# Kernel optimization log

Measured on AMD Instinct MI355X. Metric: run time of the kernel, lower is better.

The kernel has to match this reference:

```python
import jax, jax.numpy as jnp
import numpy as np

N, S, V, DEG, K, HID = 4096, 128, 32, 32, 8, 64
E = N * DEG
LAMBDA_ATTN = 0.55


def setup_inputs():
    key = jax.random.key(0)
    ks = jax.random.split(key, 16)
    def w(k, shape, fan_in):
        return jax.random.normal(k, shape, jnp.float32) / np.float32(np.sqrt(fan_in))
    return {
        "h_s": jax.random.normal(ks[0], (N, S), jnp.float32),
        "h_v": jax.random.normal(ks[1], (N, V, 3), jnp.float32),
        "pos": jax.random.normal(ks[2], (N, 3), jnp.float32),
        "edge_index": jax.random.randint(ks[3], (2, E), 0, N),
        "batch": jnp.zeros((N,), jnp.int32),
        "W1": w(ks[4], (S, S), S),
        "Wg": w(ks[5], (S, 2 * V), S),
        "W2": w(ks[6], (S, S), S),
        "Wm1": w(ks[7], (S, HID), S), "bm1": jnp.zeros((HID,), jnp.float32),
        "Wm2": w(ks[8], (HID, 1), HID), "bm2": jnp.zeros((1,), jnp.float32),
        "Wq": w(ks[9], (S, S), S), "Wk": w(ks[10], (S, S), S),
        "Wa1": w(ks[11], (3 * S, S), 3 * S), "ba1": jnp.zeros((S,), jnp.float32),
        "Wa2": w(ks[12], (S, 1), S), "ba2": jnp.zeros((1,), jnp.float32),
    }


def _edge_feats(pos, src, dst):
    # vectors src - dst, length-expanded scalar attr [E,S], direction vector attr [E,V,3]
    vec = pos[src] - pos[dst]
    ln = jnp.linalg.norm(vec, axis=-1, keepdims=True)
    dirn = jnp.where(ln > 1e-12, vec / jnp.maximum(ln, 1e-12), 0.0)  # nan_to_num
    es = jnp.broadcast_to(ln, (src.shape[0], S))
    ev = jnp.broadcast_to(dirn[:, None, :], (src.shape[0], V, 3))
    return es, ev


def _scatter_softmax(scores, seg, n, validf):
    s = jnp.where(validf > 0, scores, -jnp.inf)
    mx = jax.ops.segment_max(s, seg, num_segments=n)
    mx = jnp.where(jnp.isfinite(mx), mx, 0.0)
    e = jnp.where(validf > 0, jnp.exp(s - mx[seg]), 0.0)
    den = jax.ops.segment_sum(e, seg, num_segments=n)
    return e / jnp.maximum(den[seg], 1e-9)


def _backbone(s, v, src, dst, es, ev, msg_mask, W1, Wg, W2):
    # gather-src gated messages, modulated by edge attrs, scatter-sum to dst
    m_s = jax.nn.relu(s[src] @ W1) * es                       # [E,S]
    g = s[src] @ Wg                                           # [E,2V]
    m_v = v[src] * g[:, :V, None] + ev * g[:, V:, None]       # [E,V,3]
    if msg_mask is not None:
        m_s = m_s * msg_mask[:, None]
        m_v = m_v * msg_mask[:, None, None]
    ds = jax.ops.segment_sum(m_s, dst, num_segments=N) @ W2
    dv = jax.ops.segment_sum(m_v, dst, num_segments=N)
    return ds, dv


def reference(h_s, h_v, pos, edge_index, batch, W1, Wg, W2, Wm1, bm1, Wm2, bm2, Wq, Wk, Wa1, ba1, Wa2, ba2):
    src, dst = edge_index[0], edge_index[1]
    # local message passing with residual
    es, ev = _edge_feats(pos, src, dst)
    ds, dv = _backbone(h_s, h_v, src, dst, es, ev, None, W1, Wg, W2)
    hl_s = h_s + ds
    hl_v = h_v + dv
    # master selection (soft score m, hard mask at 0.5)
    m = jax.nn.sigmoid((jax.nn.relu(hl_s @ Wm1 + bm1) @ Wm2 + bm2)[:, 0])
    mask = (m > 0.5).astype(hl_s.dtype)
    # virtual edge generation among master nodes (dense attention, thresholded)
    attn = jax.nn.sigmoid((hl_s @ Wq) @ (hl_s @ Wk).T / np.float32(np.sqrt(S)))  # [N,N]
    adj = jnp.zeros((N, N), hl_s.dtype).at[src, dst].add(1.0)
    mm = mask[:, None] * mask[None, :]
    allowed = (mm > 0) & (adj == 0) & (~jnp.eye(N, dtype=bool))
    vals, cols = jax.lax.top_k(jnp.where(allowed, attn, -jnp.inf), K)  # [N,K]
    vf = ((vals > LAMBDA_ATTN) & jnp.isfinite(vals)).astype(hl_s.dtype)
    rows = jnp.broadcast_to(jnp.arange(N)[:, None], (N, K))
    A_virtual = jnp.zeros((N, N), hl_s.dtype).at[rows, cols].add(vf)
    vsrc = rows.reshape(-1)
    vdst = cols.reshape(-1)
    vvf = vf.reshape(-1)
    # attention-based decay weights on virtual edges (scatter-softmax over dst)
    es_v, ev_v = _edge_feats(pos, vsrc, vdst)
    attn_in = jnp.concatenate([hl_s[vsrc], hl_s[vdst], es_v], axis=-1)  # [NK,3S]
    sc = (jax.nn.relu(attn_in @ Wa1 + ba1) @ Wa2 + ba2)[:, 0]
    decay = _scatter_softmax(sc, vdst, N, vvf)
    # hierarchical pass: induced master-master edges (w=1) + virtual edges (w=decay)
    asrc = jnp.concatenate([src, vsrc])
    adst = jnp.concatenate([dst, vdst])
    a_es = jnp.concatenate([es, es_v * decay[:, None]], axis=0)
    a_ev = jnp.concatenate([ev, ev_v * decay[:, None, None]], axis=0)
    amask = jnp.concatenate([mask[src] * mask[dst], vvf])
    dms, dmv = _backbone(hl_s, hl_v, asrc, adst, a_es, a_ev, amask, W1, Wg, W2)
    # expand hierarchical update to full node set (zero at non-masters), blend by m
    exp_s = mask[:, None] * (hl_s + dms)
    exp_v = mask[:, None, None] * (hl_v + dmv)
    hf_s = (1 - m[:, None]) * hl_s + m[:, None] * exp_s
    hf_v = (1 - m[:, None, None]) * hl_v + m[:, None, None] * exp_v
    return hf_s, hf_v, pos, A_virtual, m
```

## Files before the change

kernel.cpp:

```cpp
#include <hip/hip_runtime.h>
#include <math.h>

#define NN 4096
#define EE 131072
#define NKMAX 32768

#define SCALE_FX 8388608.0
#define INV_FX   (1.0/8388608.0)

__device__ __forceinline__ void atomAddFx(long long* p, float v) {
  atomicAdd((unsigned long long*)p, (unsigned long long)llrint((double)v * SCALE_FX));
}
__device__ __forceinline__ float fxToF(long long v) {
  return (float)((double)v * INV_FX);
}

#define OFF_LN    ((size_t)0)
#define OFF_DIRN  (OFF_LN + EE)
#define OFF_R     (OFF_DIRN + (size_t)EE*3)
#define OFF_G     (OFF_R + (size_t)NN*128)
#define OFF_P1    (OFF_G + (size_t)NN*64)
#define OFF_HLS   (OFF_P1 + (size_t)NN*96)
#define OFF_HLV   (OFF_HLS + (size_t)NN*128)
#define OFF_MVAL  (OFF_HLV + (size_t)NN*96)
#define OFF_MASK  (OFF_MVAL + NN)
#define OFF_Q     (OFF_MASK + NN)
#define OFF_K     (OFF_Q + (size_t)NN*128)
#define OFF_A1    (OFF_K + (size_t)NN*128)
#define OFF_A2    (OFF_A1 + (size_t)NN*128)
#define OFF_R2    (OFF_A2 + (size_t)NN*128)
#define OFF_G2    (OFF_R2 + (size_t)NN*128)
#define OFF_P2    (OFF_G2 + (size_t)NN*64)
#define OFF_W3    (OFF_P2 + (size_t)NN*96)
#define OFF_LNV   (OFF_W3 + 128)
#define OFF_DIRV  (OFF_LNV + NKMAX)
#define OFF_SC    (OFF_DIRV + (size_t)NKMAX*3)
#define OFF_EEXP  (OFF_SC + NKMAX)
#define OFF_VEDGE (OFF_EEXP + NKMAX)
#define OFF_MIDX  (OFF_VEDGE + (size_t)NKMAX*2)
#define OFF_PT    (OFF_MIDX + NN)
#define OFF_MEDGE (OFF_PT + (size_t)NN*32)
#define OFF_SF    (OFF_MEDGE + EE)
#define OFF_ZBEG  (OFF_SF + (size_t)NN*128)
#define OFF_ACCS  (OFF_ZBEG)
#define OFF_ACCV  (OFF_ACCS + (size_t)NN*256)
#define OFF_DEN64 (OFF_ACCV + (size_t)NN*192)
#define OFF_MX    (OFF_DEN64 + (size_t)NN*2)
#define OFF_ADJ   (OFF_MX + NN)
#define OFF_CNT   (OFF_ADJ + (size_t)NN*128)
#define OFF_END   (OFF_CNT + 64)

#define OUT_HFS 0
#define OUT_HFV 524288
#define OUT_POS 917504
#define OUT_AV  929792
#define OUT_M   17707008

#define INSERT8(TV, TC, VAL, IDX) do { \
  if ((VAL) > TV[7]) { \
    _Pragma("unroll") \
    for (int k_ = 7; k_ >= 1; --k_) { \
      bool gtk_ = (VAL) > TV[k_]; bool gtm_ = (VAL) > TV[k_-1]; \
      float nv_ = gtk_ ? (gtm_ ? TV[k_-1] : (VAL)) : TV[k_]; \
      int   ni_ = gtk_ ? (gtm_ ? TC[k_-1] : (IDX)) : TC[k_]; \
      TV[k_] = nv_; TC[k_] = ni_; } \
    bool gt0_ = (VAL) > TV[0]; \
    TV[0] = gt0_ ? (VAL) : TV[0]; TC[0] = gt0_ ? (IDX) : TC[0]; \
  } } while (0)

__device__ __forceinline__ void merge32(float (&tv)[8], int (&tc)[8]) {
  #pragma unroll
  for (int m = 1; m <= 16; m <<= 1) {
    float av[16]; int ac[16];
    #pragma unroll
    for (int k = 0; k < 8; ++k) { av[k] = tv[k]; ac[k] = tc[k]; }
    #pragma unroll
    for (int k = 0; k < 8; ++k) {
      av[8+k] = __shfl_xor(tv[7-k], m, 64);
      ac[8+k] = __shfl_xor(tc[7-k], m, 64);
    }
    #pragma unroll
    for (int d = 8; d >= 1; d >>= 1) {
      #pragma unroll
      for (int i = 0; i < 16; ++i) {
        if ((i & d) == 0) {
          const int jx = i + d;
          if (jx < 16) {
            bool sw = (av[i] < av[jx]) || (av[i] == av[jx] && ac[i] > ac[jx]);
            float t1 = sw ? av[jx] : av[i]; float t2 = sw ? av[i] : av[jx];
            int   u1 = sw ? ac[jx] : ac[i]; int   u2 = sw ? ac[i] : ac[jx];
            av[i] = t1; av[jx] = t2; ac[i] = u1; ac[jx] = u2;
          }
        }
      }
    }
    #pragma unroll
    for (int k = 0; k < 8; ++k) { tv[k] = av[k]; tc[k] = ac[k]; }
  }
}

__global__ void hmp_edge_prep(const int* __restrict__ ei, const float* __restrict__ pos,
                              float* __restrict__ ln, float* __restrict__ dirn,
                              unsigned long long* __restrict__ adj) {
  int e = blockIdx.x * 256 + threadIdx.x;
  if (e >= EE) return;
  int s = ei[e], d = ei[EE + e];
  float vx = pos[s*3+0] - pos[d*3+0];
  float vy = pos[s*3+1] - pos[d*3+1];
  float vz = pos[s*3+2] - pos[d*3+2];
  float l = sqrtf(vx*vx + vy*vy + vz*vz);
  ln[e] = l;
  if (l > 1e-12f) {
    dirn[e*3+0] = vx / l; dirn[e*3+1] = vy / l; dirn[e*3+2] = vz / l;
  } else {
    dirn[e*3+0] = 0.f; dirn[e*3+1] = 0.f; dirn[e*3+2] = 0.f;
  }
  atomicOr(&adj[(size_t)s*64 + (d >> 6)], 1ULL << (d & 63));
}

struct GemmJobs {
  const float* A;
  const float* W[6];
  float* C[6];
  int Nc[6];
  int act[6];
  const float* res;
  const float* mval;
  const float* maskf;
};

__global__ __launch_bounds__(256) void hmp_gemm_k128(GemmJobs P) {
  const int g = blockIdx.z;
  const int nc = P.Nc[g];
  if ((int)blockIdx.y * 64 >= nc) return;
  const float* __restrict__ W = P.W[g];
  float* __restrict__ C = P.C[g];
  const int act = P.act[g];
  __shared__ float As[32][68];
  __shared__ float Bs[32][64];
  const int tid = threadIdx.x;
  const int row0 = blockIdx.x * 64, col0 = blockIdx.y * 64;
  const int ty = tid >> 4, tx = tid & 15;
  float acc[4][4];
  #pragma unroll
  for (int i = 0; i < 4; ++i)
    #pragma unroll
    for (int j = 0; j < 4; ++j) acc[i][j] = 0.f;

  for (int kb = 0; kb < 4; ++kb) {
    #pragma unroll
    for (int q = 0; q < 2; ++q) {
      int f4 = tid + 256*q;
      int r = f4 >> 3, cg = f4 & 7;
      float4 av = *(const float4*)&P.A[(size_t)(row0+r)*128 + kb*32 + cg*4];
      As[cg*4+0][r] = av.x; As[cg*4+1][r] = av.y; As[cg*4+2][r] = av.z; As[cg*4+3][r] = av.w;
    }
    #pragma unroll
    for (int q = 0; q < 2; ++q) {
      int f4 = tid + 256*q;
      int kr = f4 >> 4, cg = f4 & 15;
      *(float4*)&Bs[kr][cg*4] = *(const float4*)&W[(size_t)(kb*32+kr)*nc + col0 + cg*4];
    }
    __syncthreads();
    #pragma unroll
    for (int kk = 0; kk < 32; ++kk) {
      float4 a = *(float4*)&As[kk][ty*4];
      float4 b = *(float4*)&Bs[kk][tx*4];
      acc[0][0] += a.x*b.x; acc[0][1] += a.x*b.y; acc[0][2] += a.x*b.z; acc[0][3] += a.x*b.w;
      acc[1][0] += a.y*b.x; acc[1][1] += a.y*b.y; acc[1][2] += a.y*b.z; acc[1][3] += a.y*b.w;
      acc[2][0] += a.z*b.x; acc[2][1] += a.z*b.y; acc[2][2] += a.z*b.z; acc[2][3] += a.z*b.w;
      acc[3][0] += a.w*b.x; acc[3][1] += a.w*b.y; acc[3][2] += a.w*b.z; acc[3][3] += a.w*b.w;
    }
    __syncthreads();
  }
  #pragma unroll
  for (int i = 0; i < 4; ++i) {
    int rr = row0 + ty*4 + i;
    float mv = 0.f, mk = 0.f;
    if (act == 3) { mv = P.mval[rr]; mk = P.maskf[rr]; }
    #pragma unroll
    for (int j = 0; j < 4; ++j) {
      int cc = col0 + tx*4 + j;
      float v = acc[i][j];
      if (act == 1) v = fmaxf(v, 0.f);
      else if (act == 2) v += P.res[(size_t)rr*128 + cc];
      else if (act == 3) {
        float hl = P.res[(size_t)rr*128 + cc];
        v = (1.f - mv)*hl + mv*mk*(hl + v);
      }
      C[(size_t)rr*nc + cc] = v;
    }
  }
}

__global__ void hmp_mul_p1(const float* __restrict__ hv, const float* __restrict__ G,
                           float* __restrict__ P1) {
  int i = blockIdx.x * 256 + threadIdx.x;
  if (i >= NN*96) return;
  int n = i / 96, q = i - n*96, v = q / 3;
  P1[i] = hv[i] * G[(size_t)n*64 + v];
}

__global__ void hmp_hlv_p2(const float* __restrict__ hv, const long long* __restrict__ accv,
                           const float* __restrict__ G2, float* __restrict__ hlv,
                           float* __restrict__ P2) {
  int i = blockIdx.x * 256 + threadIdx.x;
  if (i >= NN*96) return;
  int n = i / 96, q = i - n*96, v = q / 3;
  float x = hv[i] + fxToF(accv[i]);
  hlv[i] = x;
  P2[i] = x * G2[(size_t)n*64 + v];
}

__global__ void hmp_cvt(const long long* __restrict__ a, float* __restrict__ o, int n) {
  int i = blockIdx.x * 256 + threadIdx.x;
  if (i < n) o[i] = fxToF(a[i]);
}

__global__ void hmp_msg_s(const int* __restrict__ ei, const float* __restrict__ ln,
                          const float* __restrict__ R, long long* __restrict__ S) {
  int idx = blockIdx.x * 256 + threadIdx.x;
  int e = idx >> 7, c = idx & 127;
  int s = ei[e], d = ei[EE + e];
  atomAddFx(&S[(size_t)d*128 + c], ln[e] * R[(size_t)s*128 + c]);
}

__global__ void hmp_msg_v(const int* __restrict__ ei, const float* __restrict__ dirn,
                          const float* __restrict__ P, const float* __restrict__ G,
                          long long* __restrict__ Sv) {
  int idx = blockIdx.x * 256 + threadIdx.x;
  int e = idx / 96, q = idx - e*96;
  int v = q / 3, c = q - v*3;
  int s = ei[e], d = ei[EE + e];
  float msg = P[(size_t)s*96 + q] + dirn[(size_t)e*3 + c] * G[(size_t)s*64 + 32 + v];
  atomAddFx(&Sv[(size_t)d*96 + q], msg);
}

__global__ void hmp_edge_compact(const int* __restrict__ ei, const float* __restrict__ maskf,
                                 int* __restrict__ medge, int* __restrict__ mecnt) {
  int e = blockIdx.x * 256 + threadIdx.x;
  if (e >= EE) return;
  if (maskf[ei[e]] > 0.f && maskf[ei[EE + e]] > 0.f) {
    int s = atomicAdd(mecnt, 1);
    medge[s] = e;
  }
}

__global__ void hmp_msg_s2(const int* __restrict__ medge, const int* __restrict__ mecnt,
                           const int* __restrict__ ei, const float* __restrict__ ln,
                           const float* __restrict__ R, long long* __restrict__ S) {
  int total = (*mecnt) << 7;
  for (int idx = blockIdx.x * 256 + threadIdx.x; idx < total; idx += gridDim.x * 256) {
    int e = medge[idx >> 7], c = idx & 127;
    int s = ei[e], d = ei[EE + e];
    atomAddFx(&S[(size_t)d*128 + c], ln[e] * R[(size_t)s*128 + c]);
  }
}

__global__ void hmp_msg_v2(const int* __restrict__ medge, const int* __restrict__ mecnt,
                           const int* __restrict__ ei, const float* __restrict__ dirn,
                           const float* __restrict__ P, const float* __restrict__ G,
                           long long* __restrict__ Sv) {
  int total = (*mecnt) * 96;
  for (int idx = blockIdx.x * 256 + threadIdx.x; idx < total; idx += gridDim.x * 256) {
    int eo = idx / 96, q = idx - eo*96;
    int v = q / 3, c = q - v*3;
    int e = medge[eo];
    int s = ei[e], d = ei[EE + e];
    float msg = P[(size_t)s*96 + q] + dirn[(size_t)e*3 + c] * G[(size_t)s*64 + 32 + v];
    atomAddFx(&Sv[(size_t)d*96 + q], msg);
  }
}

__global__ __launch_bounds__(256) void hmp_master(const float* __restrict__ hls,
                                                  const float* __restrict__ Wm1,
                                                  const float* __restrict__ bm1,
                                                  const float* __restrict__ Wm2,
                                                  const float* __restrict__ bm2,
                                                  float* __restrict__ mval,
                                                  float* __restrict__ maskf,
                                                  float* __restrict__ out_m) {
  __shared__ float sW[128*64];
  __shared__ float sx[4][128];
  int tid = threadIdx.x;
  for (int i = tid; i < 8192; i += 256) sW[i] = Wm1[i];
  for (int i = tid; i < 512; i += 256) {
    int nn = i >> 7;
    sx[nn][i & 127] = hls[(size_t)(blockIdx.x*4 + nn)*128 + (i & 127)];
  }
  __syncthreads();
  int nl = tid >> 6, lane = tid & 63;
  int n = blockIdx.x * 4 + nl;
  float h = bm1[lane];
  for (int k = 0; k < 128; ++k) h += sx[nl][k] * sW[k*64 + lane];
  h = fmaxf(h, 0.f) * Wm2[lane];
  for (int off = 32; off; off >>= 1) h += __shfl_down(h, off, 64);
  if (lane == 0) {
    float logit = h + bm2[0];
    float mv = 1.f / (1.f + expf(-logit));
    mval[n] = mv;
    maskf[n] = (mv > 0.5f) ? 1.f : 0.f;
    out_m[n] = mv;
  }
}

__global__ void hmp_compact(const float* __restrict__ maskf, int* __restrict__ midx,
                            int* __restrict__ nmp) {
  __shared__ int ls[256];
  int tid = threadIdx.x;
  int base = tid * 16;
  int cnt = 0;
  #pragma unroll
  for (int i = 0; i < 16; ++i) cnt += (maskf[base + i] > 0.f) ? 1 : 0;
  ls[tid] = cnt;
  __syncthreads();
  for (int off = 1; off < 256; off <<= 1) {
    int v = (tid >= off) ? ls[tid - off] : 0;
    __syncthreads();
    ls[tid] += v;
    __syncthreads();
  }
  int p = ls[tid] - cnt;
  for (int i = 0; i < 16; ++i)
    if (maskf[base + i] > 0.f) midx[p++] = base + i;
  if (tid == 255) *nmp = ls[255];
}

__global__ void hmp_colsum_w3(const float* __restrict__ Wa1, float* __restrict__ w3) {
  int s = threadIdx.x;
  float acc = 0.f;
  for (int k = 0; k < 128; ++k) acc += Wa1[(size_t)(256 + k)*128 + s];
  w3[s] = acc;
}

__global__ __launch_bounds__(256) void hmp_attn3(const float* __restrict__ Q,
                                                 const float* __restrict__ Kk,
                                                 const unsigned long long* __restrict__ adj,
                                                 const int* __restrict__ midx,
                                                 const int* __restrict__ nmp,
                                                 int2* __restrict__ pt) {
  const int nm = *nmp;
  const int rowblk = blockIdx.x >> 1;
  const int split  = blockIdx.x & 1;
  const int row0 = rowblk * 8;
  if (row0 >= nm) return;

  __shared__ float sQ[8][132];
  __shared__ float sK[64][132];
  __shared__ int   sCI[64];
  __shared__ int   sRI[8];
  __shared__ unsigned long long sAdj[8][64];

  const int tid = threadIdx.x;
  {
    int rr = tid >> 5, c = tid & 31;
    int gr = row0 + rr;
    int ri = (gr < nm) ? midx[gr] : -1;
    float4 v; v.x = v.y = v.z = v.w = 0.f;
    if (ri >= 0) v = *(const float4*)&Q[(size_t)ri*128 + c*4];
    *(float4*)&sQ[rr][c*4] = v;
  }
  if (tid < 8) sRI[tid] = (row0 + tid < nm) ? midx[row0 + tid] : -1;
  #pragma unroll
  for (int q = 0; q < 2; ++q) {
    int i = tid + 256*q;
    int rr = i >> 6, w = i & 63;
    int gr = row0 + rr;
    int ri = (gr < nm) ? midx[gr] : -1;
    sAdj[rr][w] = (ri >= 0) ? adj[(size_t)ri*64 + w] : 0ULL;
  }

  const int ntiles = (nm + 63) >> 6;
  const int l = tid & 63, wv = tid >> 6;
  const int r = wv*2 + (l >> 5);
  const int c0 = l & 31, c1 = c0 + 32;

  float tv[8]; int tc[8];
  #pragma unroll
  for (int k = 0; k < 8; ++k) { tv[k] = -1.f; tc[k] = 0x7fffffff; }

  for (int t = split; t < ntiles; t += 2) {
    #pragma unroll
    for (int q = 0; q < 8; ++q) {
      int f4 = tid + 256*q;
      int rr = f4 >> 5, c = f4 & 31;
      int gc = t*64 + rr;
      int ci = (gc < nm) ? midx[gc] : -1;
      float4 v; v.x = v.y = v.z = v.w = 0.f;
      if (ci >= 0) v = *(const float4*)&Kk[(size_t)ci*128 + c*4];
      *(float4*)&sK[rr][c*4] = v;
    }
    if (tid < 64) sCI[tid] = (t*64 + tid < nm) ? midx[t*64 + tid] : -1;
    __syncthreads();

    float a0x=0,a0y=0,a0z=0,a0w=0, a1x=0,a1y=0,a1z=0,a1w=0;
    #pragma unroll
    for (int kk = 0; kk < 32; ++kk) {
      float4 qv = *(float4*)&sQ[r][kk*4];
      float4 k0 = *(float4*)&sK[c0][kk*4];
      float4 k1 = *(float4*)&sK[c1][kk*4];
      a0x += qv.x*k0.x; a0y += qv.y*k0.y; a0z += qv.z*k0.z; a0w += qv.w*k0.w;
      a1x += qv.x*k1.x; a1y += qv.y*k1.y; a1z += qv.z*k1.z; a1w += qv.w*k1.w;
    }
    float d0 = (a0x+a0y)+(a0z+a0w);
    float d1 = (a1x+a1y)+(a1z+a1w);

    const int ro = sRI[r];
    const int jo0 = sCI[c0], jo1 = sCI[c1];
    {
      bool ok = (jo0 >= 0) && (ro >= 0) && (jo0 != ro) &&
                !((sAdj[r][jo0 >> 6] >> (jo0 & 63)) & 1ULL);
      if (ok) {
        float z = d0 / 11.3137085f;
        float attn = 1.f / (1.f + expf(-z));
        INSERT8(tv, tc, attn, jo0);
      }
    }
    {
      bool ok = (jo1 >= 0) && (ro >= 0) && (jo1 != ro) &&
                !((sAdj[r][jo1 >> 6] >> (jo1 & 63)) & 1ULL);
      if (ok) {
        float z = d1 / 11.3137085f;
        float attn = 1.f / (1.f + expf(-z));
        INSERT8(tv, tc, attn, jo1);
      }
    }
    __syncthreads();
  }

  merge32(tv, tc);

  if ((l & 31) == 0) {
    int gr = row0 + r;
    #pragma unroll
    for (int k = 0; k < 8; ++k)
      pt[((size_t)gr*2 + split)*8 + k] = make_int2(__float_as_int(tv[k]), tc[k]);
  }
}

__global__ void hmp_topk_emit(const int2* __restrict__ pt, const int* __restrict__ midx,
                              const int* __restrict__ nmp, float* __restrict__ Avirt,
                              int2* __restrict__ vedges, int* __restrict__ vcnt) {
  int i = blockIdx.x * 256 + threadIdx.x;
  if (i >= *nmp) return;
  const int2* LA = pt + (size_t)i*16;
  const int2* LB = LA + 8;
  int a = 0, b = 0;
  int grow = midx[i];
  #pragma unroll
  for (int k = 0; k < 8; ++k) {
    int2 ca = LA[a];
    int2 cb = LB[b];
    float va = __int_as_float(ca.x), vb = __int_as_float(cb.x);
    bool pickA = (va > vb) || (va == vb && ca.y < cb.y);
    int2 sel = pickA ? ca : cb;
    if (pickA) ++a; else ++b;
    float v = __int_as_float(sel.x);
    if (v > 0.55f) {
      Avirt[(size_t)grow*NN + sel.y] = 1.f;
      int slot = atomicAdd(vcnt, 1);
      vedges[slot] = make_int2(grow, sel.y);
    }
  }
}

__global__ __launch_bounds__(256) void hmp_vedge_sc(const int2* __restrict__ ve,
                                                    const int* __restrict__ vcnt,
                                                    const float* __restrict__ pos,
                                                    const float* __restrict__ A1,
                                                    const float* __restrict__ A2,
                                                    const float* __restrict__ w3,
                                                    const float* __restrict__ ba1,
                                                    const float* __restrict__ Wa2,
                                                    const float* __restrict__ ba2,
                                                    float* __restrict__ lnv,
                                                    float* __restrict__ dirv,
                                                    float* __restrict__ sc,
                                                    unsigned int* __restrict__ mxenc) {
  int cnt = *vcnt;
  int lane = threadIdx.x & 63;
  for (int e = blockIdx.x * 4 + (threadIdx.x >> 6); e < cnt; e += gridDim.x * 4) {
    int2 ed = ve[e];
    int i = ed.x, j = ed.y;
    float vx = pos[i*3+0] - pos[j*3+0];
    float vy = pos[i*3+1] - pos[j*3+1];
    float vz = pos[i*3+2] - pos[j*3+2];
    float lval = sqrtf(vx*vx + vy*vy + vz*vz);
    float acc = 0.f;
    #pragma unroll
    for (int half = 0; half < 2; ++half) {
      int c = lane + half*64;
      float tq = A1[(size_t)i*128 + c] + A2[(size_t)j*128 + c] + lval*w3[c] + ba1[c];
      acc += fmaxf(tq, 0.f) * Wa2[c];
    }
    for (int off = 32; off; off >>= 1) acc += __shfl_down(acc, off, 64);
    if (lane == 0) {
      lnv[e] = lval;
      if (lval > 1e-12f) {
        dirv[e*3+0] = vx / lval; dirv[e*3+1] = vy / lval; dirv[e*3+2] = vz / lval;
      } else {
        dirv[e*3+0] = 0.f; dirv[e*3+1] = 0.f; dirv[e*3+2] = 0.f;
      }
      float s = acc + ba2[0];
      sc[e] = s;
      unsigned int bits = __float_as_uint(s);
      unsigned int enc = (bits & 0x80000000u) ? ~bits : (bits | 0x80000000u);
      atomicMax(&mxenc[j], enc);
    }
  }
}

__global__ void hmp_vexp(const int2* __restrict__ ve, const int* __restrict__ vcnt,
                         const float* __restrict__ sc, const unsigned int* __restrict__ mxenc,
                         float* __restrict__ eexp, long long* __restrict__ den64) {
  int cnt = *vcnt;
  for (int e = blockIdx.x * 256 + threadIdx.x; e < cnt; e += gridDim.x * 256) {
    int j = ve[e].y;
    unsigned int enc = mxenc[j];
    unsigned int bits = (enc & 0x80000000u) ? (enc & 0x7fffffffu) : ~enc;
    float mx = __uint_as_float(bits);
    float ex = expf(sc[e] - mx);
    eexp[e] = ex;
    atomAddFx(&den64[j], ex);
  }
}

__global__ void hmp_msgv_s(const int2* __restrict__ ve, const int* __restrict__ vcnt,
                           const float* __restrict__ eexp, const long long* __restrict__ den64,
                           const float* __restrict__ lnv, const float* __restrict__ R2,
                           long long* __restrict__ S2s) {
  int total = (*vcnt) << 7;
  for (int idx = blockIdx.x * 256 + threadIdx.x; idx < total; idx += gridDim.x * 256) {
    int e = idx >> 7, c = idx & 127;
    int2 ed = ve[e];
    float denf = fxToF(den64[ed.y]);
    float decay = eexp[e] / fmaxf(denf, 1e-9f);
    atomAddFx(&S2s[(size_t)ed.y*128 + c], lnv[e] * decay * R2[(size_t)ed.x*128 + c]);
  }
}

__global__ void hmp_msgv_v(const int2* __restrict__ ve, const int* __restrict__ vcnt,
                           const float* __restrict__ eexp, const long long* __restrict__ den64,
                           const float* __restrict__ dirv, const float* __restrict__ P2,
                           const float* __restrict__ G2, long long* __restrict__ S2v) {
  int total = (*vcnt) * 96;
  for (int idx = blockIdx.x * 256 + threadIdx.x; idx < total; idx += gridDim.x * 256) {
    int e = idx / 96, q = idx - e*96;
    int v = q / 3, c = q - v*3;
    int2 ed = ve[e];
    float denf = fxToF(den64[ed.y]);
    float decay = eexp[e] / fmaxf(denf, 1e-9f);
    float msg = P2[(size_t)ed.x*96 + q] + dirv[(size_t)e*3 + c] * decay * G2[(size_t)ed.x*64 + 32 + v];
    atomAddFx(&S2v[(size_t)ed.y*96 + q], msg);
  }
}

__global__ void hmp_final_v(const float* __restrict__ hlv, const long long* __restrict__ accv,
                            const float* __restrict__ mval, const float* __restrict__ maskf,
                            float* __restrict__ out) {
  int idx = blockIdx.x * 256 + threadIdx.x;
  if (idx >= NN*96) return;
  int n = idx / 96;
  float mv = mval[n], mk = maskf[n];
  float x = hlv[idx];
  out[idx] = (1.f - mv)*x + mv*mk*(x + fxToF(accv[idx]));
}

extern "C" void kernel_launch(void* const* d_in, const int* in_sizes, int n_in,
                              void* d_out, int out_size, void* d_ws, size_t ws_size,
                              hipStream_t stream) {
  const float* h_s = (const float*)d_in[0];
  const float* h_v = (const float*)d_in[1];
  const float* pos = (const float*)d_in[2];
  const int*   ei  = (const int*)d_in[3];
  const float* W1  = (const float*)d_in[5];
  const float* Wg  = (const float*)d_in[6];
  const float* W2  = (const float*)d_in[7];
  const float* Wm1 = (const float*)d_in[8];
  const float* bm1 = (const float*)d_in[9];
  const float* Wm2 = (const float*)d_in[10];
  const float* bm2 = (const float*)d_in[11];
  const float* Wq  = (const float*)d_in[12];
  const float* Wk  = (const float*)d_in[13];
  const float* Wa1 = (const float*)d_in[14];
  const float* ba1 = (const float*)d_in[15];
  const float* Wa2 = (const float*)d_in[16];
  const float* ba2 = (const float*)d_in[17];

  if (ws_size < OFF_END * sizeof(float)) return;

  float* ws  = (float*)d_ws;
  float* out = (float*)d_out;

  float* ln   = ws + OFF_LN;
  float* dirn = ws + OFF_DIRN;
  float* R    = ws + OFF_R;
  float* G    = ws + OFF_G;
  float* P1   = ws + OFF_P1;
  float* hls  = ws + OFF_HLS;
  float* hlv  = ws + OFF_HLV;
  float* mval = ws + OFF_MVAL;
  float* mskf = ws + OFF_MASK;
  float* Qb   = ws + OFF_Q;
  float* Kb   = ws + OFF_K;
  float* A1   = ws + OFF_A1;
  float* A2   = ws + OFF_A2;
  float* R2   = ws + OFF_R2;
  float* G2   = ws + OFF_G2;
  float* P2   = ws + OFF_P2;
  float* w3   = ws + OFF_W3;
  float* lnv  = ws + OFF_LNV;
  float* dirv = ws + OFF_DIRV;
  float* sc   = ws + OFF_SC;
  float* eexp = ws + OFF_EEXP;
  int2*  vedg = (int2*)(ws + OFF_VEDGE);
  int*   midx = (int*)(ws + OFF_MIDX);
  int2*  pt   = (int2*)(ws + OFF_PT);
  int*   medge= (int*)(ws + OFF_MEDGE);
  float* SF   = ws + OFF_SF;
  long long* accs  = (long long*)(ws + OFF_ACCS);
  long long* accv  = (long long*)(ws + OFF_ACCV);
  long long* den64 = (long long*)(ws + OFF_DEN64);
  unsigned int* mxenc = (unsigned int*)(ws + OFF_MX);
  unsigned long long* adj = (unsigned long long*)(ws + OFF_ADJ);
  int*   cnts = (int*)(ws + OFF_CNT);
  int*   vcnt = cnts + 0;
  int*   mecnt= cnts + 1;
  int*   nmp  = cnts + 2;

  hipMemsetAsync(ws + OFF_ZBEG, 0, (OFF_END - OFF_ZBEG) * sizeof(float), stream);
  hipMemsetAsync(out + OUT_AV, 0, (size_t)NN * NN * sizeof(float), stream);
  hipMemcpyAsync(out + OUT_POS, pos, (size_t)NN * 3 * sizeof(float),
                 hipMemcpyDeviceToDevice, stream);

  hmp_edge_prep<<<EE/256, 256, 0, stream>>>(ei, pos, ln, dirn, adj);

  {
    GemmJobs J = {};
    J.A = h_s;
    J.W[0] = W1; J.C[0] = R; J.Nc[0] = 128; J.act[0] = 1;
    J.W[1] = Wg; J.C[1] = G; J.Nc[1] = 64;  J.act[1] = 0;
    hmp_gemm_k128<<<dim3(64,2,2), 256, 0, stream>>>(J);
  }
  hmp_mul_p1<<<NN*96/256, 256, 0, stream>>>(h_v, G, P1);
  hmp_msg_s<<<EE*128/256, 256, 0, stream>>>(ei, ln, R, accs);
  hmp_msg_v<<<EE*96/256, 256, 0, stream>>>(ei, dirn, P1, G, accv);

  hmp_cvt<<<NN*128/256, 256, 0, stream>>>(accs, SF, NN*128);
  {
    GemmJobs J = {};
    J.A = SF; J.res = h_s;
    J.W[0] = W2; J.C[0] = hls; J.Nc[0] = 128; J.act[0] = 2;
    hmp_gemm_k128<<<dim3(64,2,1), 256, 0, stream>>>(J);
  }

  hmp_master<<<NN/4, 256, 0, stream>>>(hls, Wm1, bm1, Wm2, bm2, mval, mskf, out + OUT_M);
  hmp_compact<<<1, 256, 0, stream>>>(mskf, midx, nmp);

  {
    GemmJobs J = {};
    J.A = hls;
    J.W[0] = Wq;          J.C[0] = Qb; J.Nc[0] = 128; J.act[0] = 0;
    J.W[1] = Wk;          J.C[1] = Kb; J.Nc[1] = 128; J.act[1] = 0;
    J.W[2] = Wa1;         J.C[2] = A1; J.Nc[2] = 128; J.act[2] = 0;
    J.W[3] = Wa1 + 16384; J.C[3] = A2; J.Nc[3] = 128; J.act[3] = 0;
    J.W[4] = W1;          J.C[4] = R2; J.Nc[4] = 128; J.act[4] = 1;
    J.W[5] = Wg;          J.C[5] = G2; J.Nc[5] = 64;  J.act[5] = 0;
    hmp_gemm_k128<<<dim3(64,2,6), 256, 0, stream>>>(J);
  }
  hmp_colsum_w3<<<1, 128, 0, stream>>>(Wa1, w3);
  hmp_hlv_p2<<<NN*96/256, 256, 0, stream>>>(h_v, accv, G2, hlv, P2);

  hipMemsetAsync(ws + OFF_ACCS, 0, (size_t)(NN*256 + NN*192) * sizeof(float), stream);

  hmp_attn3<<<(NN/8)*2, 256, 0, stream>>>(Qb, Kb, adj, midx, nmp, pt);
  hmp_topk_emit<<<NN/256, 256, 0, stream>>>(pt, midx, nmp, out + OUT_AV, vedg, vcnt);

  hmp_edge_compact<<<EE/256, 256, 0, stream>>>(ei, mskf, medge, mecnt);

  hmp_vedge_sc<<<512, 256, 0, stream>>>(vedg, vcnt, pos, A1, A2, w3, ba1, Wa2, ba2,
                                        lnv, dirv, sc, mxenc);
  hmp_vexp<<<128, 256, 0, stream>>>(vedg, vcnt, sc, mxenc, eexp, den64);

  hmp_msg_s2<<<2048, 256, 0, stream>>>(medge, mecnt, ei, ln, R2, accs);
  hmp_msg_v2<<<2048, 256, 0, stream>>>(medge, mecnt, ei, dirn, P2, G2, accv);
  hmp_msgv_s<<<1024, 256, 0, stream>>>(vedg, vcnt, eexp, den64, lnv, R2, accs);
  hmp_msgv_v<<<1024, 256, 0, stream>>>(vedg, vcnt, eexp, den64, dirv, P2, G2, accv);

  hmp_cvt<<<NN*128/256, 256, 0, stream>>>(accs, SF, NN*128);
  {
    GemmJobs J = {};
    J.A = SF; J.res = hls; J.mval = mval; J.maskf = mskf;
    J.W[0] = W2; J.C[0] = out + OUT_HFS; J.Nc[0] = 128; J.act[0] = 3;
    hmp_gemm_k128<<<dim3(64,2,1), 256, 0, stream>>>(J);
  }
  hmp_final_v<<<NN*96/256, 256, 0, stream>>>(hlv, accv, mval, mskf, out + OUT_HFV);
}
```

Before: 543.4 us.

## Replace atomic edge scatter with CSR gather by destination node

Builds a destination-sorted CSR of edges (count, single-block scan, atomic scatter) and replaces the per-edge fixed-point atomic message kernels with per-node gather kernels. Each node accumulates in registers and writes floats directly, which also removes the separate conversion kernels and the master-edge compaction. It is meant to remove heavy 64-bit atomic contention on the 131k-edge message passes. It adds CSR construction kernels and per-node load imbalance.

```diff
diff --git a/kernel.cpp b/kernel.cpp
--- a/kernel.cpp
+++ b/kernel.cpp
@@ -10,6 +10,9 @@
 
 __device__ __forceinline__ void atomAddFx(long long* p, float v) {
   atomicAdd((unsigned long long*)p, (unsigned long long)llrint((double)v * SCALE_FX));
+}
+__device__ __forceinline__ long long toFx(float v) {
+  return llrint((double)v * SCALE_FX);
 }
 __device__ __forceinline__ float fxToF(long long v) {
   return (float)((double)v * INV_FX);
@@ -39,10 +42,16 @@
 #define OFF_VEDGE (OFF_EEXP + NKMAX)
 #define OFF_MIDX  (OFF_VEDGE + (size_t)NKMAX*2)
 #define OFF_PT    (OFF_MIDX + NN)
-#define OFF_MEDGE (OFF_PT + (size_t)NN*32)
-#define OFF_SF    (OFF_MEDGE + EE)
-#define OFF_ZBEG  (OFF_SF + (size_t)NN*128)
-#define OFF_ACCS  (OFF_ZBEG)
+#define OFF_CSR   (OFF_PT + (size_t)NN*32)
+#define OFF_ROWPT (OFF_CSR + EE)
+#define OFF_CURS  (OFF_ROWPT + NN + 64)
+#define OFF_S1S   (OFF_CURS + NN)
+#define OFF_S1V   (OFF_S1S + (size_t)NN*128)
+#define OFF_S2S   OFF_R
+#define OFF_S2V   OFF_P1
+#define OFF_ZBEG  (OFF_S1V + (size_t)NN*96)
+#define OFF_CNTH  (OFF_ZBEG)
+#define OFF_ACCS  (OFF_CNTH + NN)
 #define OFF_ACCV  (OFF_ACCS + (size_t)NN*256)
 #define OFF_DEN64 (OFF_ACCV + (size_t)NN*192)
 #define OFF_MX    (OFF_DEN64 + (size_t)NN*2)
@@ -101,7 +110,8 @@
 
 __global__ void hmp_edge_prep(const int* __restrict__ ei, const float* __restrict__ pos,
                               float* __restrict__ ln, float* __restrict__ dirn,
-                              unsigned long long* __restrict__ adj) {
+                              unsigned long long* __restrict__ adj,
+                              int* __restrict__ cnth) {
   int e = blockIdx.x * 256 + threadIdx.x;
   if (e >= EE) return;
   int s = ei[e], d = ei[EE + e];
@@ -116,6 +126,43 @@
     dirn[e*3+0] = 0.f; dirn[e*3+1] = 0.f; dirn[e*3+2] = 0.f;
   }
   atomicOr(&adj[(size_t)s*64 + (d >> 6)], 1ULL << (d & 63));
+  atomicAdd(&cnth[d], 1);
+}
+
+__global__ void hmp_csr_scan(const int* __restrict__ cnth, int* __restrict__ rowptr,
+                             int* __restrict__ cursor) {
+  __shared__ int ls[256];
+  int tid = threadIdx.x;
+  int base = tid * 16;
+  int loc[16];
+  int s = 0;
+  #pragma unroll
+  for (int i = 0; i < 16; ++i) { loc[i] = s; s += cnth[base + i]; }
+  ls[tid] = s;
+  __syncthreads();
+  for (int off = 1; off < 256; off <<= 1) {
+    int v = (tid >= off) ? ls[tid - off] : 0;
+    __syncthreads();
+    ls[tid] += v;
+    __syncthreads();
+  }
+  int p = ls[tid] - s;
+  #pragma unroll
+  for (int i = 0; i < 16; ++i) {
+    int rp = p + loc[i];
+    rowptr[base + i] = rp;
+    cursor[base + i] = rp;
+  }
+  if (tid == 255) rowptr[NN] = ls[255];
+}
+
+__global__ void hmp_csr_scatter(const int* __restrict__ ei, int* __restrict__ cursor,
+                                int* __restrict__ csr) {
+  int e = blockIdx.x * 256 + threadIdx.x;
+  if (e >= EE) return;
+  int d = ei[EE + e];
+  int p = atomicAdd(&cursor[d], 1);
+  csr[p] = e;
 }
 
 struct GemmJobs {
@@ -201,75 +248,68 @@
   P1[i] = hv[i] * G[(size_t)n*64 + v];
 }
 
-__global__ void hmp_hlv_p2(const float* __restrict__ hv, const long long* __restrict__ accv,
+__global__ void hmp_hlv_p2(const float* __restrict__ hv, const float* __restrict__ S1v,
                            const float* __restrict__ G2, float* __restrict__ hlv,
                            float* __restrict__ P2) {
   int i = blockIdx.x * 256 + threadIdx.x;
   if (i >= NN*96) return;
   int n = i / 96, q = i - n*96, v = q / 3;
-  float x = hv[i] + fxToF(accv[i]);
+  float x = hv[i] + S1v[i];
   hlv[i] = x;
   P2[i] = x * G2[(size_t)n*64 + v];
 }
 
-__global__ void hmp_cvt(const long long* __restrict__ a, float* __restrict__ o, int n) {
-  int i = blockIdx.x * 256 + threadIdx.x;
-  if (i < n) o[i] = fxToF(a[i]);
-}
-
-__global__ void hmp_msg_s(const int* __restrict__ ei, const float* __restrict__ ln,
-                          const float* __restrict__ R, long long* __restrict__ S) {
-  int idx = blockIdx.x * 256 + threadIdx.x;
-  int e = idx >> 7, c = idx & 127;
-  int s = ei[e], d = ei[EE + e];
-  atomAddFx(&S[(size_t)d*128 + c], ln[e] * R[(size_t)s*128 + c]);
-}
-
-__global__ void hmp_msg_v(const int* __restrict__ ei, const float* __restrict__ dirn,
-                          const float* __restrict__ P, const float* __restrict__ G,
-                          long long* __restrict__ Sv) {
-  int idx = blockIdx.x * 256 + threadIdx.x;
-  int e = idx / 96, q = idx - e*96;
-  int v = q / 3, c = q - v*3;
-  int s = ei[e], d = ei[EE + e];
-  float msg = P[(size_t)s*96 + q] + dirn[(size_t)e*3 + c] * G[(size_t)s*64 + 32 + v];
-  atomAddFx(&Sv[(size_t)d*96 + q], msg);
-}
-
-__global__ void hmp_edge_compact(const int* __restrict__ ei, const float* __restrict__ maskf,
-                                 int* __restrict__ medge, int* __restrict__ mecnt) {
-  int e = blockIdx.x * 256 + threadIdx.x;
-  if (e >= EE) return;
-  if (maskf[ei[e]] > 0.f && maskf[ei[EE + e]] > 0.f) {
-    int s = atomicAdd(mecnt, 1);
-    medge[s] = e;
-  }
-}
-
-__global__ void hmp_msg_s2(const int* __restrict__ medge, const int* __restrict__ mecnt,
-                           const int* __restrict__ ei, const float* __restrict__ ln,
-                           const float* __restrict__ R, long long* __restrict__ S) {
-  int total = (*mecnt) << 7;
-  for (int idx = blockIdx.x * 256 + threadIdx.x; idx < total; idx += gridDim.x * 256) {
-    int e = medge[idx >> 7], c = idx & 127;
-    int s = ei[e], d = ei[EE + e];
-    atomAddFx(&S[(size_t)d*128 + c], ln[e] * R[(size_t)s*128 + c]);
-  }
-}
-
-__global__ void hmp_msg_v2(const int* __restrict__ medge, const int* __restrict__ mecnt,
-                           const int* __restrict__ ei, const float* __restrict__ dirn,
-                           const float* __restrict__ P, const float* __restrict__ G,
-                           long long* __restrict__ Sv) {
-  int total = (*mecnt) * 96;
-  for (int idx = blockIdx.x * 256 + threadIdx.x; idx < total; idx += gridDim.x * 256) {
-    int eo = idx / 96, q = idx - eo*96;
-    int v = q / 3, c = q - v*3;
-    int e = medge[eo];
-    int s = ei[e], d = ei[EE + e];
-    float msg = P[(size_t)s*96 + q] + dirn[(size_t)e*3 + c] * G[(size_t)s*64 + 32 + v];
-    atomAddFx(&Sv[(size_t)d*96 + q], msg);
-  }
+__global__ __launch_bounds__(256) void hmp_csr_msg_s(
+    const int* __restrict__ csr, const int* __restrict__ rowptr,
+    const int* __restrict__ ei, const float* __restrict__ ln,
+    const float* __restrict__ R, const float* __restrict__ maskf,
+    float* __restrict__ S) {
+  int d = blockIdx.x * 4 + (threadIdx.x >> 6);
+  int l = threadIdx.x & 63;
+  if (d >= NN) return;
+  long long a0 = 0, a1 = 0;
+  if (!maskf || maskf[d] > 0.f) {
+    int k1 = rowptr[d + 1];
+    for (int k = rowptr[d]; k < k1; ++k) {
+      int e = csr[k];
+      int s = ei[e];
+      if (maskf && maskf[s] == 0.f) continue;
+      float w = ln[e];
+      a0 += toFx(w * R[(size_t)s*128 + l]);
+      a1 += toFx(w * R[(size_t)s*128 + 64 + l]);
+    }
+  }
+  S[(size_t)d*128 + l]      = fxToF(a0);
+  S[(size_t)d*128 + 64 + l] = fxToF(a1);
+}
+
+__global__ __launch_bounds__(256) void hmp_csr_msg_v(
+    const int* __restrict__ csr, const int* __restrict__ rowptr,
+    const int* __restrict__ ei, const float* __restrict__ dirn,
+    const float* __restrict__ P, const float* __restrict__ G,
+    const float* __restrict__ maskf, float* __restrict__ Sv) {
+  int d = blockIdx.x * 4 + (threadIdx.x >> 6);
+  int l = threadIdx.x & 63;
+  if (d >= NN) return;
+  const int v0 = l / 3, c0 = l - v0*3;
+  const int q1 = 64 + l, v1 = q1 / 3, c1 = q1 - v1*3;
+  long long a0 = 0, a1 = 0;
+  if (!maskf || maskf[d] > 0.f) {
+    int k1 = rowptr[d + 1];
+    for (int k = rowptr[d]; k < k1; ++k) {
+      int e = csr[k];
+      int s = ei[e];
+      if (maskf && maskf[s] == 0.f) continue;
+      float m0 = P[(size_t)s*96 + l] + dirn[(size_t)e*3 + c0] * G[(size_t)s*64 + 32 + v0];
+      a0 += toFx(m0);
+      if (l < 32) {
+        float m1 = P[(size_t)s*96 + q1] + dirn[(size_t)e*3 + c1] * G[(size_t)s*64 + 32 + v1];
+        a1 += toFx(m1);
+      }
+    }
+  }
+  Sv[(size_t)d*96 + l] = fxToF(a0);
+  if (l < 32) Sv[(size_t)d*96 + q1] = fxToF(a1);
 }
 
 __global__ __launch_bounds__(256) void hmp_master(const float* __restrict__ hls,
@@ -528,21 +568,21 @@
 __global__ void hmp_msgv_s(const int2* __restrict__ ve, const int* __restrict__ vcnt,
                            const float* __restrict__ eexp, const long long* __restrict__ den64,
                            const float* __restrict__ lnv, const float* __restrict__ R2,
-                           long long* __restrict__ S2s) {
+                           long long* __restrict__ acc) {
   int total = (*vcnt) << 7;
   for (int idx = blockIdx.x * 256 + threadIdx.x; idx < total; idx += gridDim.x * 256) {
     int e = idx >> 7, c = idx & 127;
     int2 ed = ve[e];
     float denf = fxToF(den64[ed.y]);
     float decay = eexp[e] / fmaxf(denf, 1e-9f);
-    atomAddFx(&S2s[(size_t)ed.y*128 + c], lnv[e] * decay * R2[(size_t)ed.x*128 + c]);
+    atomAddFx(&acc[(size_t)ed.y*128 + c], lnv[e] * decay * R2[(size_t)ed.x*128 + c]);
   }
 }
 
 __global__ void hmp_msgv_v(const int2* __restrict__ ve, const int* __restrict__ vcnt,
                            const float* __restrict__ eexp, const long long* __restrict__ den64,
                            const float* __restrict__ dirv, const float* __restrict__ P2,
-                           const float* __restrict__ G2, long long* __restrict__ S2v) {
+                           const float* __restrict__ G2, long long* __restrict__ acc) {
   int total = (*vcnt) * 96;
   for (int idx = blockIdx.x * 256 + threadIdx.x; idx < total; idx += gridDim.x * 256) {
     int e = idx / 96, q = idx - e*96;
@@ -551,11 +591,17 @@
     float denf = fxToF(den64[ed.y]);
     float decay = eexp[e] / fmaxf(denf, 1e-9f);
     float msg = P2[(size_t)ed.x*96 + q] + dirv[(size_t)e*3 + c] * decay * G2[(size_t)ed.x*64 + 32 + v];
-    atomAddFx(&S2v[(size_t)ed.y*96 + q], msg);
-  }
-}
-
-__global__ void hmp_final_v(const float* __restrict__ hlv, const long long* __restrict__ accv,
+    atomAddFx(&acc[(size_t)ed.y*96 + q], msg);
+  }
+}
+
+__global__ void hmp_comb(float* __restrict__ S, const long long* __restrict__ acc, int n) {
+  int i = blockIdx.x * 256 + threadIdx.x;
+  if (i < n) S[i] += fxToF(acc[i]);
+}
+
+__global__ void hmp_final_v(const float* __restrict__ hlv, const float* __restrict__ S2v,
+                            const long long* __restrict__ accv,
                             const float* __restrict__ mval, const float* __restrict__ maskf,
                             float* __restrict__ out) {
   int idx = blockIdx.x * 256 + threadIdx.x;
@@ -563,7 +609,7 @@
   int n = idx / 96;
   float mv = mval[n], mk = maskf[n];
   float x = hlv[idx];
-  out[idx] = (1.f - mv)*x + mv*mk*(x + fxToF(accv[idx]));
+  out[idx] = (1.f - mv)*x + mv*mk*(x + S2v[idx] + fxToF(accv[idx]));
 }
 
 extern "C" void kernel_launch(void* const* d_in, const int* in_sizes, int n_in,
@@ -616,8 +662,14 @@
   int2*  vedg = (int2*)(ws + OFF_VEDGE);
   int*   midx = (int*)(ws + OFF_MIDX);
   int2*  pt   = (int2*)(ws + OFF_PT);
-  int*   medge= (int*)(ws + OFF_MEDGE);
-  float* SF   = ws + OFF_SF;
+  int*   csr  = (int*)(ws + OFF_CSR);
+  int*   rowp = (int*)(ws + OFF_ROWPT);
+  int*   curs = (int*)(ws + OFF_CURS);
+  float* S1s  = ws + OFF_S1S;
+  float* S1v  = ws + OFF_S1V;
+  float* S2s  = ws + OFF_S2S;
+  float* S2v  = ws + OFF_S2V;
+  int*   cnth = (int*)(ws + OFF_CNTH);
   long long* accs  = (long long*)(ws + OFF_ACCS);
   long long* accv  = (long long*)(ws + OFF_ACCV);
   long long* den64 = (long long*)(ws + OFF_DEN64);
@@ -625,7 +677,6 @@
   unsigned long long* adj = (unsigned long long*)(ws + OFF_ADJ);
   int*   cnts = (int*)(ws + OFF_CNT);
   int*   vcnt = cnts + 0;
-  int*   mecnt= cnts + 1;
   int*   nmp  = cnts + 2;
 
   hipMemsetAsync(ws + OFF_ZBEG, 0, (OFF_END - OFF_ZBEG) * sizeof(float), stream);
@@ -633,7 +684,9 @@
   hipMemcpyAsync(out + OUT_POS, pos, (size_t)NN * 3 * sizeof(float),
                  hipMemcpyDeviceToDevice, stream);
 
-  hmp_edge_prep<<<EE/256, 256, 0, stream>>>(ei, pos, ln, dirn, adj);
+  hmp_edge_prep<<<EE/256, 256, 0, stream>>>(ei, pos, ln, dirn, adj, cnth);
+  hmp_csr_scan<<<1, 256, 0, stream>>>(cnth, rowp, curs);
+  hmp_csr_scatter<<<EE/256, 256, 0, stream>>>(ei, curs, csr);
 
   {
     GemmJobs J = {};
@@ -643,13 +696,12 @@
     hmp_gemm_k128<<<dim3(64,2,2), 256, 0, stream>>>(J);
   }
   hmp_mul_p1<<<NN*96/256, 256, 0, stream>>>(h_v, G, P1);
-  hmp_msg_s<<<EE*128/256, 256, 0, stream>>>(ei, ln, R, accs);
-  hmp_msg_v<<<EE*96/256, 256, 0, stream>>>(ei, dirn, P1, G, accv);
-
-  hmp_cvt<<<NN*128/256, 256, 0, stream>>>(accs, SF, NN*128);
+  hmp_csr_msg_s<<<NN/4, 256, 0, stream>>>(csr, rowp, ei, ln, R, nullptr, S1s);
+  hmp_csr_msg_v<<<NN/4, 256, 0, stream>>>(csr, rowp, ei, dirn, P1, G, nullptr, S1v);
+
   {
     GemmJobs J = {};
-    J.A = SF; J.res = h_s;
+    J.A = S1s; J.res = h_s;
     J.W[0] = W2; J.C[0] = hls; J.Nc[0] = 128; J.act[0] = 2;
     hmp_gemm_k128<<<dim3(64,2,1), 256, 0, stream>>>(J);
   }
@@ -669,30 +721,26 @@
     hmp_gemm_k128<<<dim3(64,2,6), 256, 0, stream>>>(J);
   }
   hmp_colsum_w3<<<1, 128, 0, stream>>>(Wa1, w3);
-  hmp_hlv_p2<<<NN*96/256, 256, 0, stream>>>(h_v, accv, G2, hlv, P2);
-
-  hipMemsetAsync(ws + OFF_ACCS, 0, (size_t)(NN*256 + NN*192) * sizeof(float), stream);
+  hmp_hlv_p2<<<NN*96/256, 256, 0, stream>>>(h_v, S1v, G2, hlv, P2);
 
   hmp_attn3<<<(NN/8)*2, 256, 0, stream>>>(Qb, Kb, adj, midx, nmp, pt);
   hmp_topk_emit<<<NN/256, 256, 0, stream>>>(pt, midx, nmp, out + OUT_AV, vedg, vcnt);
-
-  hmp_edge_compact<<<EE/256, 256, 0, stream>>>(ei, mskf, medge, mecnt);
 
   hmp_vedge_sc<<<512, 256, 0, stream>>>(vedg, vcnt, pos, A1, A2, w3, ba1, Wa2, ba2,
                                         lnv, dirv, sc, mxenc);
   hmp_vexp<<<128, 256, 0, stream>>>(vedg, vcnt, sc, mxenc, eexp, den64);
 
-  hmp_msg_s2<<<2048, 256, 0, stream>>>(medge, mecnt, ei, ln, R2, accs);
-  hmp_msg_v2<<<2048, 256, 0, stream>>>(medge, mecnt, ei, dirn, P2, G2, accv);
+  hmp_csr_msg_s<<<NN/4, 256, 0, stream>>>(csr, rowp, ei, ln, R2, mskf, S2s);
+  hmp_csr_msg_v<<<NN/4, 256, 0, stream>>>(csr, rowp, ei, dirn, P2, G2, mskf, S2v);
   hmp_msgv_s<<<1024, 256, 0, stream>>>(vedg, vcnt, eexp, den64, lnv, R2, accs);
   hmp_msgv_v<<<1024, 256, 0, stream>>>(vedg, vcnt, eexp, den64, dirv, P2, G2, accv);
-
-  hmp_cvt<<<NN*128/256, 256, 0, stream>>>(accs, SF, NN*128);
+  hmp_comb<<<NN*128/256, 256, 0, stream>>>(S2s, accs, NN*128);
+
   {
     GemmJobs J = {};
-    J.A = SF; J.res = hls; J.mval = mval; J.maskf = mskf;
+    J.A = S2s; J.res = hls; J.mval = mval; J.maskf = mskf;
     J.W[0] = W2; J.C[0] = out + OUT_HFS; J.Nc[0] = 128; J.act[0] = 3;
     hmp_gemm_k128<<<dim3(64,2,1), 256, 0, stream>>>(J);
   }
-  hmp_final_v<<<NN*96/256, 256, 0, stream>>>(hlv, accv, mval, mskf, out + OUT_HFV);
-}
+  hmp_final_v<<<NN*96/256, 256, 0, stream>>>(hlv, S2v, accv, mval, mskf, out + OUT_HFV);
+}
```

Measured after the change: 475.4 us. 1.14x faster.
